# Kernel optimization log

Measured on AMD Instinct MI355X. Metric: run time of the kernel, lower is better.

Reference implementation:

```python
import jax, jax.numpy as jnp
import numpy as np

N, E, D = 100000, 1600000, 128
EPS = 1e-5


def _bn(h, g, b):
    m = h.mean(0)
    v = ((h - m) ** 2).mean(0)  # biased var, as torch BatchNorm1d normalization
    return g * (h - m) / jnp.sqrt(v + EPS) + b


def _sage(x, src, dst, w_self, w_neigh, b, n):
    # mean aggregation over in-neighbors (edges src->dst)
    agg = jax.ops.segment_sum(x[src], dst, num_segments=n)          # [N, D]
    cnt = jax.ops.segment_sum(jnp.ones(src.shape, x.dtype), dst, num_segments=n)
    mean = agg / jnp.maximum(cnt, 1.0)[:, None]
    return x @ w_self + mean @ w_neigh + b


def setup_inputs() -> dict:
    key = jax.random.key(0)
    ks = jax.random.split(key, 8)
    s = 1.0 / np.sqrt(D)
    return {
        "x": jax.random.normal(ks[0], (N, D), jnp.float32),
        "src": jax.random.randint(ks[1], (E,), 0, N, jnp.int32),
        "dst": jax.random.randint(ks[2], (E,), 0, N, jnp.int32),
        "w_self1": jax.random.normal(ks[3], (D, D), jnp.float32) * s,
        "w_neigh1": jax.random.normal(ks[4], (D, D), jnp.float32) * s,
        "b1": jnp.zeros((D,), jnp.float32),
        "w_self2": jax.random.normal(ks[5], (D, D), jnp.float32) * s,
        "w_neigh2": jax.random.normal(ks[6], (D, D), jnp.float32) * s,
        "b2": jnp.zeros((D,), jnp.float32),
        "w_skip": jax.random.normal(ks[7], (D, D), jnp.float32) * s,
        "b_skip": jnp.zeros((D,), jnp.float32),
        "g1": jnp.ones((D,), jnp.float32), "be1": jnp.zeros((D,), jnp.float32),
        "g2": jnp.ones((D,), jnp.float32), "be2": jnp.zeros((D,), jnp.float32),
        "g3": jnp.ones((D,), jnp.float32), "be3": jnp.zeros((D,), jnp.float32),
    }


def reference(x, src, dst, w_self1, w_neigh1, b1, w_self2, w_neigh2, b2,
              w_skip, b_skip, g1, be1, g2, be2, g3, be3):
    n = x.shape[0]
    h1 = _sage(x, src, dst, w_self1, w_neigh1, b1, n)
    h1 = jax.nn.relu(_bn(h1, g1, be1))           # dropout: eval-mode identity
    h2 = _sage(h1, src, dst, w_self2, w_neigh2, b2, n)
    h2 = _bn(h2, g2, be2)
    skip = _bn(h1 @ w_skip + b_skip, g3, be3)
    return jax.nn.relu(h2 + skip)
```

## Files before the change

kernel.cpp:

```cpp
#include <hip/hip_runtime.h>

#define D 128
#define PCHUNK 4096
#define SCAP 8192

typedef short bf16x8 __attribute__((ext_vector_type(8)));
typedef float f32x4 __attribute__((ext_vector_type(4)));
typedef float f32x2 __attribute__((ext_vector_type(2)));

__device__ __forceinline__ ushort f2b(float f){
  unsigned u = __builtin_bit_cast(unsigned, f);
  u += 0x7fffu + ((u >> 16) & 1u);
  return (ushort)(u >> 16);
}
__device__ __forceinline__ float b2f(ushort h){
  unsigned u = ((unsigned)h) << 16;
  return __builtin_bit_cast(float, u);
}
__device__ __forceinline__ f32x2 upk(unsigned u){
  f32x2 r;
  r.x = __builtin_bit_cast(float, u << 16);
  r.y = __builtin_bit_cast(float, u & 0xffff0000u);
  return r;
}

__global__ __launch_bounds__(256) void k_p0(const int* __restrict__ dst,
                                            int* __restrict__ bcnt, int E){
  __shared__ int h[512];
  for (int u=threadIdx.x; u<512; u+=256) h[u]=0;
  __syncthreads();
  for (long long i=(long long)blockIdx.x*256+threadIdx.x; i<E; i+=(long long)gridDim.x*256)
    atomicAdd(&h[dst[i]>>8], 1);
  __syncthreads();
  for (int u=threadIdx.x; u<512; u+=256) if (h[u]) atomicAdd(&bcnt[u], h[u]);
}

__global__ void k_bscan(const int* __restrict__ bcnt, int* __restrict__ bbase,
                        int* __restrict__ bcur, int nb, int E){
  __shared__ int sh[1024];
  int t = threadIdx.x;
  int v = (t<nb) ? bcnt[t] : 0;
  sh[t]=v; __syncthreads();
  for (int off=1; off<1024; off<<=1){
    int add = (t>=off)?sh[t-off]:0;
    __syncthreads();
    sh[t]+=add;
    __syncthreads();
  }
  if (t<nb){ int e=sh[t]-v; bbase[t]=e; bcur[t]=e; }
  if (t==nb) bbase[t]=E;
}

__global__ __launch_bounds__(256) void k_part(const int* __restrict__ src,
        const int* __restrict__ dst, int* __restrict__ bcur,
        unsigned* __restrict__ pairs, int E){
  __shared__ int hist[512], offA[512], offB[512], gbase[512];
  __shared__ int sS[PCHUNK], sD[PCHUNK];
  const int t = threadIdx.x;
  const int base = blockIdx.x * PCHUNK;
  const int cnt = min(PCHUNK, E - base);
  for (int u=t; u<512; u+=256) hist[u]=0;
  __syncthreads();
  int rs[16], rd[16];
  #pragma unroll
  for (int j=0;j<16;j++){
    int li = j*256 + t;
    if (li < cnt){
      rs[j]=src[base+li]; rd[j]=dst[base+li];
      atomicAdd(&hist[rd[j]>>8],1);
    } else { rs[j]=0; rd[j]=-1; }
  }
  __syncthreads();
  int *cur=offA, *nxt=offB;
  for (int u=t; u<512; u+=256) cur[u]=hist[u];
  __syncthreads();
  for (int off=1; off<512; off<<=1){
    for (int u=t; u<512; u+=256) nxt[u] = cur[u] + ((u>=off)?cur[u-off]:0);
    __syncthreads();
    int* tmp=cur; cur=nxt; nxt=tmp;
  }
  for (int u=t; u<512; u+=256) nxt[u] = cur[u]-hist[u];
  __syncthreads();
  #pragma unroll
  for (int j=0;j<16;j++){
    if (j*256+t < cnt){
      int b = rd[j]>>8;
      int p = atomicAdd(&nxt[b],1);
      sS[p]=rs[j]; sD[p]=rd[j];
    }
  }
  __syncthreads();
  for (int u=t; u<512; u+=256){
    int c = hist[u];
    if (c>0) gbase[u] = atomicAdd(&bcur[u], c);
  }
  __syncthreads();
  #pragma unroll
  for (int j=0;j<16;j++){
    int idx = j*256+t;
    if (idx<cnt){
      int d = sD[idx]; int b = d>>8;
      int gpos = gbase[b] + (idx - (cur[b]-hist[b]));
      pairs[gpos] = (unsigned)sS[idx] | ((unsigned)(d & 255) << 24);
    }
  }
}

__global__ __launch_bounds__(256) void k_sortb(const unsigned* __restrict__ pairs,
        const int* __restrict__ bbase, int* __restrict__ offs,
        int* __restrict__ slots, int N, int NB){
  __shared__ int nh[256], nc[256], sc[256];
  __shared__ int stage[SCAP];
  const int b = blockIdx.x, t = threadIdx.x;
  const int base = bbase[b];
  const int cnt  = bbase[b+1] - base;
  nh[t]=0; __syncthreads();
  for (int i=t;i<cnt;i+=256) atomicAdd(&nh[pairs[base+i] >> 24],1);
  __syncthreads();
  int v = nh[t];
  sc[t]=v; __syncthreads();
  for (int off=1; off<256; off<<=1){
    int add = (t>=off)?sc[t-off]:0;
    __syncthreads();
    sc[t]+=add;
    __syncthreads();
  }
  int excl = sc[t]-v;
  nc[t]=excl;
  int node = (b<<8)+t;
  if (node<N) offs[node]=base+excl;
  if (b==NB-1 && t==0) offs[N]=bbase[NB];
  __syncthreads();
  if (cnt<=SCAP){
    for (int i=t;i<cnt;i+=256){
      unsigned p = pairs[base+i];
      int pos = atomicAdd(&nc[p >> 24],1);
      stage[pos]=(int)(p & 0xffffffu);
    }
    __syncthreads();
    for (int i=t;i<cnt;i+=256) slots[base+i]=stage[i];
  } else {
    for (int i=t;i<cnt;i+=256){
      unsigned p = pairs[base+i];
      int pos = atomicAdd(&nc[p >> 24],1);
      slots[base+pos]=(int)(p & 0xffffffu);
    }
  }
}

__global__ __launch_bounds__(256) void k_xcast(const float* __restrict__ x,
                                               ushort* __restrict__ xb, long long n4){
  long long i = (long long)blockIdx.x*256 + threadIdx.x;
  const long long stride = (long long)gridDim.x*256;
  for (; i < n4; i += stride){
    float4 v = reinterpret_cast<const float4*>(x)[i];
    ushort4 o;
    o.x = f2b(v.x); o.y = f2b(v.y); o.z = f2b(v.z); o.w = f2b(v.w);
    reinterpret_cast<ushort4*>(xb)[i] = o;
  }
}

__global__ void k_wt(const float* __restrict__ W, ushort* __restrict__ Wb, int K, int k0){
  int idx = blockIdx.x*256 + threadIdx.x;
  int k = idx >> 7, c = idx & 127;
  Wb[(size_t)c*K + k0 + k] = f2b(W[idx]);
}

__global__ __launch_bounds__(256) void k_gatherb(const ushort* __restrict__ Xb,
        const int* __restrict__ slots, const int* __restrict__ offs,
        ushort* __restrict__ meanb, int N){
  int node = blockIdx.x*4 + (threadIdx.x >> 6);
  const unsigned c2 = (threadIdx.x & 63) * 2;
  if (node >= N) return;
  const int beg = offs[node], end = offs[node+1];
  f32x2 s0{0,0},s1{0,0},s2{0,0},s3{0,0},s4{0,0},s5{0,0},s6{0,0},s7{0,0};
  int j = beg;
  while (j < end && (j & 3)){
    s0 += upk(*reinterpret_cast<const unsigned*>(Xb + ((unsigned)slots[j]*128u + c2)));
    ++j;
  }
  const int nfull = (end - j) >> 3;
  const int4* sp = reinterpret_cast<const int4*>(slots + j);

#define GLD(dstv, idx) dstv = *reinterpret_cast<const unsigned*>(Xb + ((unsigned)(idx)*128u + c2))
#define GATHER8(U, ia, ib) \
    GLD(U##0, (ia).x); GLD(U##1, (ia).y); GLD(U##2, (ia).z); GLD(U##3, (ia).w); \
    GLD(U##4, (ib).x); GLD(U##5, (ib).y); GLD(U##6, (ib).z); GLD(U##7, (ib).w)
#define ACC8(U) \
    s0 += upk(U##0); s1 += upk(U##1); s2 += upk(U##2); s3 += upk(U##3); \
    s4 += upk(U##4); s5 += upk(U##5); s6 += upk(U##6); s7 += upk(U##7)

  unsigned a0,a1,a2,a3,a4,a5,a6,a7;
  unsigned b0,b1,b2,b3,b4,b5,b6,b7;
  if (nfull > 0){
    int4 ia = sp[0], ib = sp[1];
    GATHER8(a, ia, ib);
    int g = 1;
    if (nfull > 1){ ia = sp[2]; ib = sp[3]; }
    for (; g + 1 < nfull; g += 2){
      GATHER8(b, ia, ib);
      ia = sp[2*g+2]; ib = sp[2*g+3];
      ACC8(a);
      GATHER8(a, ia, ib);
      if (g + 2 < nfull){ ia = sp[2*g+4]; ib = sp[2*g+5]; }
      ACC8(b);
    }
    if (g < nfull){
      GATHER8(b, ia, ib);
      ACC8(a);
      ACC8(b);
    } else {
      ACC8(a);
    }
  }
  j += 8*nfull;
  if (end - j >= 4){
    int4 ia = *reinterpret_cast<const int4*>(slots + j);
    unsigned t0,t1,t2,t3;
    GLD(t0, ia.x); GLD(t1, ia.y); GLD(t2, ia.z); GLD(t3, ia.w);
    s0 += upk(t0); s1 += upk(t1); s2 += upk(t2); s3 += upk(t3);
    j += 4;
  }
  for (; j < end; ++j)
    s0 += upk(*reinterpret_cast<const unsigned*>(Xb + ((unsigned)slots[j]*128u + c2)));
#undef GLD
#undef GATHER8
#undef ACC8
  f32x2 s = ((s0+s1)+(s2+s3)) + ((s4+s5)+(s6+s7));
  float deg = (float)(end - beg);
  float rc = deg > 0.f ? 1.0f/deg : 0.f;
  unsigned o = (unsigned)f2b(s.x*rc) | ((unsigned)f2b(s.y*rc) << 16);
  *reinterpret_cast<unsigned*>(meanb + ((size_t)node*D + c2)) = o;
}

template<bool SKIP>
__global__ __launch_bounds__(256, 2) void k_mfma(
    const ushort* __restrict__ A0, const ushort* __restrict__ A1,
    const ushort* __restrict__ Wb, const ushort* __restrict__ Wk,
    const float* __restrict__ bias, const float* __restrict__ biasK,
    ushort* __restrict__ C, ushort* __restrict__ Ck,
    float* __restrict__ gS, float* __restrict__ gQ,
    float* __restrict__ gSK, float* __restrict__ gQK, int N, int NT)
{
  __shared__ ushort At[2][64][40];
  __shared__ ushort Wt[2][128][40];
  __shared__ ushort Wkt[SKIP ? 2*128*40 : 1];
  __shared__ float shS[128], shQ[128], shSK[SKIP?128:1], shQK[SKIP?128:1];
  const int tid = threadIdx.x;
  if (tid < 128){ shS[tid]=0.f; shQ[tid]=0.f; if (SKIP){ shSK[tid]=0.f; shQK[tid]=0.f; } }
  const int bid = blockIdx.x, gridN = gridDim.x;
  const int lane = tid & 63, wid = tid >> 6;
  const int wr = wid >> 1, wc = wid & 1;
  const int lr = lane & 15, kq = lane >> 4;
  const int srA = tid >> 2, s8A = (tid & 3) * 8;
  const int srW = tid >> 2, s8W = (tid & 3) * 8;

  int4 va0, va1, va2, va3;
  int4 w0a,w0b, w1a,w1b, w2a,w2b, w3a,w3b;
  int4 k0a,k0b, k1a,k1b, k2a,k2b, k3a,k3b;

#define LOADSET(S, GT, TT) { \
    int grow_ = (GT)*64 + srA; if (grow_ >= N) grow_ = N-1; \
    const ushort* As_ = ((TT) >= 4) ? A1 : A0; \
    va##S = *reinterpret_cast<const int4*>(&As_[(size_t)grow_*D + ((TT)&3)*32 + s8A]); \
    w##S##a = *reinterpret_cast<const int4*>(&Wb[(size_t)srW*256 + (TT)*32 + s8W]); \
    w##S##b = *reinterpret_cast<const int4*>(&Wb[(size_t)(srW+64)*256 + (TT)*32 + s8W]); \
    if (SKIP && (TT) < 4){ \
      k##S##a = *reinterpret_cast<const int4*>(&Wk[(size_t)srW*128 + (TT)*32 + s8W]); \
      k##S##b = *reinterpret_cast<const int4*>(&Wk[(size_t)(srW+64)*128 + (TT)*32 + s8W]); \
    } }

#define WRITESET(S, BW, TT) { \
    *reinterpret_cast<int4*>(&At[BW][srA][s8A]) = va##S; \
    *reinterpret_cast<int4*>(&Wt[BW][srW][s8W]) = w##S##a; \
    *reinterpret_cast<int4*>(&Wt[BW][srW+64][s8W]) = w##S##b; \
    if (SKIP && (TT) < 4){ \
      *reinterpret_cast<int4*>(&Wkt[((BW)*128 + srW)*40 + s8W]) = k##S##a; \
      *reinterpret_cast<int4*>(&Wkt[((BW)*128 + srW + 64)*40 + s8W]) = k##S##b; \
    } }

#define PBAR() { asm volatile("s_waitcnt lgkmcnt(0)" ::: "memory"); \
    __builtin_amdgcn_s_barrier(); __builtin_amdgcn_sched_barrier(0); }

#define STEPBODY(BR, WITHK, ...) { \
    bf16x8 af0 = *reinterpret_cast<const bf16x8*>(&At[BR][32*wr + lr][kq*8]); \
    bf16x8 af1 = *reinterpret_cast<const bf16x8*>(&At[BR][32*wr + 16 + lr][kq*8]); \
    bf16x8 bw0 = *reinterpret_cast<const bf16x8*>(&Wt[BR][64*wc + lr][kq*8]); \
    bf16x8 bw1 = *reinterpret_cast<const bf16x8*>(&Wt[BR][64*wc + 16 + lr][kq*8]); \
    bf16x8 bw2 = *reinterpret_cast<const bf16x8*>(&Wt[BR][64*wc + 32 + lr][kq*8]); \
    bf16x8 bw3 = *reinterpret_cast<const bf16x8*>(&Wt[BR][64*wc + 48 + lr][kq*8]); \
    bf16x8 bk0{}, bk1{}, bk2{}, bk3{}; \
    if (SKIP && (WITHK)){ \
      bk0 = *reinterpret_cast<const bf16x8*>(&Wkt[((BR)*128 + 64*wc + lr)*40 + kq*8]); \
      bk1 = *reinterpret_cast<const bf16x8*>(&Wkt[((BR)*128 + 64*wc + 16 + lr)*40 + kq*8]); \
      bk2 = *reinterpret_cast<const bf16x8*>(&Wkt[((BR)*128 + 64*wc + 32 + lr)*40 + kq*8]); \
      bk3 = *reinterpret_cast<const bf16x8*>(&Wkt[((BR)*128 + 64*wc + 48 + lr)*40 + kq*8]); \
    } \
    __VA_ARGS__; \
    acc[0][0] = __builtin_amdgcn_mfma_f32_16x16x32_bf16(af0, bw0, acc[0][0], 0,0,0); \
    acc[0][1] = __builtin_amdgcn_mfma_f32_16x16x32_bf16(af0, bw1, acc[0][1], 0,0,0); \
    acc[0][2] = __builtin_amdgcn_mfma_f32_16x16x32_bf16(af0, bw2, acc[0][2], 0,0,0); \
    acc[0][3] = __builtin_amdgcn_mfma_f32_16x16x32_bf16(af0, bw3, acc[0][3], 0,0,0); \
    acc[1][0] = __builtin_amdgcn_mfma_f32_16x16x32_bf16(af1, bw0, acc[1][0], 0,0,0); \
    acc[1][1] = __builtin_amdgcn_mfma_f32_16x16x32_bf16(af1, bw1, acc[1][1], 0,0,0); \
    acc[1][2] = __builtin_amdgcn_mfma_f32_16x16x32_bf16(af1, bw2, acc[1][2], 0,0,0); \
    acc[1][3] = __builtin_amdgcn_mfma_f32_16x16x32_bf16(af1, bw3, acc[1][3], 0,0,0); \
    if (SKIP && (WITHK)){ \
      accK[0][0] = __builtin_amdgcn_mfma_f32_16x16x32_bf16(af0, bk0, accK[0][0], 0,0,0); \
      accK[0][1] = __builtin_amdgcn_mfma_f32_16x16x32_bf16(af0, bk1, accK[0][1], 0,0,0); \
      accK[0][2] = __builtin_amdgcn_mfma_f32_16x16x32_bf16(af0, bk2, accK[0][2], 0,0,0); \
      accK[0][3] = __builtin_amdgcn_mfma_f32_16x16x32_bf16(af0, bk3, accK[0][3], 0,0,0); \
      accK[1][0] = __builtin_amdgcn_mfma_f32_16x16x32_bf16(af1, bk0, accK[1][0], 0,0,0); \
      accK[1][1] = __builtin_amdgcn_mfma_f32_16x16x32_bf16(af1, bk1, accK[1][1], 0,0,0); \
      accK[1][2] = __builtin_amdgcn_mfma_f32_16x16x32_bf16(af1, bk2, accK[1][2], 0,0,0); \
      accK[1][3] = __builtin_amdgcn_mfma_f32_16x16x32_bf16(af1, bk3, accK[1][3], 0,0,0); \
    } }

  f32x4 acc[2][4], accK[SKIP?2:1][SKIP?4:1];
  #pragma unroll
  for (int m=0;m<2;m++)
    #pragma unroll
    for (int n=0;n<4;n++){
      acc[m][n] = (f32x4){0.f,0.f,0.f,0.f};
      if (SKIP) accK[m][n] = (f32x4){0.f,0.f,0.f,0.f};
    }
  float bs[4]={0,0,0,0}, bq[4]={0,0,0,0}, bsk[4]={0,0,0,0}, bqk[4]={0,0,0,0};
  float bv[4], bkv[4];
  #pragma unroll
  for (int n=0;n<4;n++){
    bv[n] = bias[64*wc + 16*n + lr];
    bkv[n] = SKIP ? biasK[64*wc + 16*n + lr] : 0.f;
  }

  {
    const int t0 = bid;
    LOADSET(0, t0, 0);
    LOADSET(1, t0, 1);
    LOADSET(2, t0, 2);
    LOADSET(3, t0, 3);
    WRITESET(0, 0, 0);
    PBAR();
  }

  for (int tile = bid; tile < NT; tile += gridN){
    const int tnext = tile + gridN;
    const bool hasnext = (tnext < NT);
    STEPBODY(0, 1, LOADSET(0, tile, 4));
    WRITESET(1, 1, 1); PBAR();
    STEPBODY(1, 1, LOADSET(1, tile, 5));
    WRITESET(2, 0, 2); PBAR();
    STEPBODY(0, 1, LOADSET(2, tile, 6));
    WRITESET(3, 1, 3); PBAR();
    STEPBODY(1, 1, LOADSET(3, tile, 7));
    WRITESET(0, 0, 4); PBAR();
    STEPBODY(0, 0, if (hasnext) LOADSET(0, tnext, 0));
    WRITESET(1, 1, 5); PBAR();
    STEPBODY(1, 0, if (hasnext) LOADSET(1, tnext, 1));
    WRITESET(2, 0, 6); PBAR();
    STEPBODY(0, 0, if (hasnext) LOADSET(2, tnext, 2));
    WRITESET(3, 1, 7); PBAR();
    STEPBODY(1, 0, if (hasnext) LOADSET(3, tnext, 3));
    if (hasnext){ WRITESET(0, 0, 0); PBAR(); }

    #pragma unroll
    for (int m=0;m<2;m++){
      #pragma unroll
      for (int r=0;r<4;r++){
        int row = tile*64 + 32*wr + 16*m + kq*4 + r;
        if (row < N){
          #pragma unroll
          for (int n=0;n<4;n++){
            int col = 64*wc + 16*n + lr;
            float v = acc[m][n][r] + bv[n];
            C[(size_t)row*D + col] = f2b(v);
            bs[n] += v; bq[n] += v*v;
            if (SKIP){
              float u = accK[m][n][r] + bkv[n];
              Ck[(size_t)row*D + col] = f2b(u);
              bsk[n] += u; bqk[n] += u*u;
            }
          }
        }
      }
    }
    #pragma unroll
    for (int m=0;m<2;m++)
      #pragma unroll
      for (int n=0;n<4;n++){
        acc[m][n] = (f32x4){0.f,0.f,0.f,0.f};
        if (SKIP) accK[m][n] = (f32x4){0.f,0.f,0.f,0.f};
      }
  }
#undef LOADSET
#undef WRITESET
#undef PBAR
#undef STEPBODY

  #pragma unroll
  for (int n=0;n<4;n++){
    float s = bs[n], q = bq[n];
    s += __shfl_xor(s,16); s += __shfl_xor(s,32);
    q += __shfl_xor(q,16); q += __shfl_xor(q,32);
    if (kq == 0){
      int col = 64*wc + 16*n + lr;
      atomicAdd(&shS[col], s);
      atomicAdd(&shQ[col], q);
    }
    if (SKIP){
      float sk = bsk[n], qk = bqk[n];
      sk += __shfl_xor(sk,16); sk += __shfl_xor(sk,32);
      qk += __shfl_xor(qk,16); qk += __shfl_xor(qk,32);
      if (kq == 0){
        int col = 64*wc + 16*n + lr;
        atomicAdd(&shSK[col], sk);
        atomicAdd(&shQK[col], qk);
      }
    }
  }
  __syncthreads();
  if (tid < 128){
    unsafeAtomicAdd(&gS[tid], shS[tid]);
    unsafeAtomicAdd(&gQ[tid], shQ[tid]);
    if (SKIP){
      unsafeAtomicAdd(&gSK[tid], shSK[tid]);
      unsafeAtomicAdd(&gQK[tid], shQK[tid]);
    }
  }
}

__global__ void k_bnfin(const float* __restrict__ sum, const float* __restrict__ sq,
                        const float* __restrict__ g, const float* __restrict__ be,
                        float* __restrict__ bnA, float* __restrict__ bnB, float invN){
  int c = threadIdx.x;
  float m = sum[c]*invN;
  float v = sq[c]*invN - m*m;
  float a = g[c]*rsqrtf(fmaxf(v, 0.f) + 1e-5f);
  bnA[c] = a;
  bnB[c] = be[c] - m*a;
}

__global__ __launch_bounds__(256) void k_bnrelub(const ushort* __restrict__ hpre,
      ushort* __restrict__ hb,
      const float* __restrict__ A, const float* __restrict__ Bp, long long n4){
  long long i = (long long)blockIdx.x*256 + threadIdx.x;
  const long long stride = (long long)gridDim.x*256;
  for (; i < n4; i += stride){
    int c = ((int)(i & 31)) << 2;
    float4 a = *reinterpret_cast<const float4*>(A + c);
    float4 b = *reinterpret_cast<const float4*>(Bp + c);
    ushort4 hv = reinterpret_cast<const ushort4*>(hpre)[i];
    ushort4 o;
    o.x = f2b(fmaxf(a.x*b2f(hv.x) + b.x, 0.f));
    o.y = f2b(fmaxf(a.y*b2f(hv.y) + b.y, 0.f));
    o.z = f2b(fmaxf(a.z*b2f(hv.z) + b.z, 0.f));
    o.w = f2b(fmaxf(a.w*b2f(hv.w) + b.w, 0.f));
    reinterpret_cast<ushort4*>(hb)[i] = o;
  }
}

__global__ __launch_bounds__(256) void k_final(const ushort* __restrict__ h2,
      const ushort* __restrict__ sk, float* __restrict__ out,
      const float* __restrict__ A2, const float* __restrict__ B2,
      const float* __restrict__ A3, const float* __restrict__ B3, long long n4){
  long long i = (long long)blockIdx.x*256 + threadIdx.x;
  const long long stride = (long long)gridDim.x*256;
  for (; i < n4; i += stride){
    int c = ((int)(i & 31)) << 2;
    float4 a2 = *reinterpret_cast<const float4*>(A2 + c);
    float4 b2 = *reinterpret_cast<const float4*>(B2 + c);
    float4 a3 = *reinterpret_cast<const float4*>(A3 + c);
    float4 b3 = *reinterpret_cast<const float4*>(B3 + c);
    ushort4 h = reinterpret_cast<const ushort4*>(h2)[i];
    ushort4 s = reinterpret_cast<const ushort4*>(sk)[i];
    float4 v;
    v.x = fmaxf(a2.x*b2f(h.x) + b2.x + a3.x*b2f(s.x) + b3.x, 0.f);
    v.y = fmaxf(a2.y*b2f(h.y) + b2.y + a3.y*b2f(s.y) + b3.y, 0.f);
    v.z = fmaxf(a2.z*b2f(h.z) + b2.z + a3.z*b2f(s.z) + b3.z, 0.f);
    v.w = fmaxf(a2.w*b2f(h.w) + b2.w + a3.w*b2f(s.w) + b3.w, 0.f);
    reinterpret_cast<float4*>(out)[i] = v;
  }
}

extern "C" void kernel_launch(void* const* d_in, const int* in_sizes, int n_in,
                              void* d_out, int out_size, void* d_ws, size_t ws_size,
                              hipStream_t stream) {
  const float* x        = (const float*)d_in[0];
  const int*   src      = (const int*)  d_in[1];
  const int*   dst      = (const int*)  d_in[2];
  const float* w_self1  = (const float*)d_in[3];
  const float* w_neigh1 = (const float*)d_in[4];
  const float* b1       = (const float*)d_in[5];
  const float* w_self2  = (const float*)d_in[6];
  const float* w_neigh2 = (const float*)d_in[7];
  const float* b2       = (const float*)d_in[8];
  const float* w_skip   = (const float*)d_in[9];
  const float* b_skip   = (const float*)d_in[10];
  const float* g1       = (const float*)d_in[11];
  const float* be1      = (const float*)d_in[12];
  const float* g2       = (const float*)d_in[13];
  const float* be2      = (const float*)d_in[14];
  const float* g3       = (const float*)d_in[15];
  const float* be3      = (const float*)d_in[16];
  (void)n_in; (void)ws_size;

  const int N = in_sizes[0] / D;
  const int E = in_sizes[1];
  const int NB = (N + 255) >> 8;
  float* out = (float*)d_out;

  char* p = (char*)d_ws;
  const size_t nd2 = (((size_t)N * D * 2) + 255) / 256 * 256;
  ushort* meanb  = (ushort*)p; p += nd2;
  ushort* h1b    = (ushort*)p; p += nd2;
  ushort* hpre_b = (ushort*)p; p += nd2;
  ushort* skip_b = (ushort*)p; p += nd2;
  ushort* Wb1    = (ushort*)p; p += 256*128*2;
  ushort* Wb2    = (ushort*)p; p += 256*128*2;
  ushort* Wb3    = (ushort*)p; p += 128*128*2;
  int*    offs   = (int*)p;   p += (((size_t)(N+1)*4) + 255) / 256 * 256;
  int*    bcnt   = (int*)p;   p += 2304;
  float*  st     = (float*)p; p += 1536*sizeof(float);
  int*    bbase  = (int*)p;   p += 2304;
  int*    bcur   = (int*)p;   p += 2048;
  float *sum1=st,      *sq1=st+128,  *sum2=st+256, *sq2=st+384, *sum3=st+512, *sq3=st+640;
  float *bnA1=st+768,  *bnB1=st+896, *bnA2=st+1024,*bnB2=st+1152,*bnA3=st+1280,*bnB3=st+1408;

  const size_t slpad = (((size_t)E*4) + 255) / 256 * 256;
  const size_t xbpad = (((size_t)N*D*2) + 255) / 256 * 256;
  int*      slots = (int*)d_out;
  ushort*   xb    = (ushort*)((char*)d_out + slpad);
  unsigned* pairs = (unsigned*)((char*)d_out + slpad + xbpad);

  hipMemsetAsync(bcnt, 0, 2304 + 1536*sizeof(float), stream);

  const long long n4 = (long long)N * D / 4;

  k_xcast<<<2048, 256, 0, stream>>>(x, xb, n4);
  k_wt<<<64, 256, 0, stream>>>(w_self1,  Wb1, 256, 0);
  k_wt<<<64, 256, 0, stream>>>(w_neigh1, Wb1, 256, 128);
  k_wt<<<64, 256, 0, stream>>>(w_self2,  Wb2, 256, 0);
  k_wt<<<64, 256, 0, stream>>>(w_neigh2, Wb2, 256, 128);
  k_wt<<<64, 256, 0, stream>>>(w_skip,   Wb3, 128, 0);

  k_p0<<<1024, 256, 0, stream>>>(dst, bcnt, E);
  k_bscan<<<1, 1024, 0, stream>>>(bcnt, bbase, bcur, NB, E);
  k_part<<<(E + PCHUNK - 1)/PCHUNK, 256, 0, stream>>>(src, dst, bcur, pairs, E);
  k_sortb<<<NB, 256, 0, stream>>>(pairs, bbase, offs, slots, N, NB);

  const int gablocks = (N + 3) / 4;
  const int NT = (N + 63) / 64;
  const int gpersist = 512;
  const float invN = 1.0f / (float)N;

  k_gatherb<<<gablocks, 256, 0, stream>>>(xb, slots, offs, meanb, N);
  k_mfma<false><<<gpersist, 256, 0, stream>>>(xb, meanb, Wb1, nullptr, b1, nullptr,
                                              hpre_b, nullptr, sum1, sq1, nullptr, nullptr, N, NT);
  k_bnfin<<<1, 128, 0, stream>>>(sum1, sq1, g1, be1, bnA1, bnB1, invN);
  k_bnrelub<<<4096, 256, 0, stream>>>(hpre_b, h1b, bnA1, bnB1, n4);

  k_gatherb<<<gablocks, 256, 0, stream>>>(h1b, slots, offs, meanb, N);

  k_mfma<true><<<gpersist, 256, 0, stream>>>(h1b, meanb, Wb2, Wb3, b2, b_skip,
                                             hpre_b, skip_b, sum2, sq2, sum3, sq3, N, NT);
  k_bnfin<<<1, 128, 0, stream>>>(sum2, sq2, g2, be2, bnA2, bnB2, invN);
  k_bnfin<<<1, 128, 0, stream>>>(sum3, sq3, g3, be3, bnA3, bnB3, invN);

  k_final<<<4096, 256, 0, stream>>>(hpre_b, skip_b, out, bnA2, bnB2, bnA3, bnB3, n4);
}
```

Before: 343.6 us.

## Split neighbor gather across feature slices and edge lanes with shuffle reduction

```diff
diff --git a/kernel.cpp b/kernel.cpp
--- a/kernel.cpp
+++ b/kernel.cpp
@@ -6,7 +6,6 @@
 
 typedef short bf16x8 __attribute__((ext_vector_type(8)));
 typedef float f32x4 __attribute__((ext_vector_type(4)));
-typedef float f32x2 __attribute__((ext_vector_type(2)));
 
 __device__ __forceinline__ ushort f2b(float f){
   unsigned u = __builtin_bit_cast(unsigned, f);
@@ -16,12 +15,6 @@
 __device__ __forceinline__ float b2f(ushort h){
   unsigned u = ((unsigned)h) << 16;
   return __builtin_bit_cast(float, u);
-}
-__device__ __forceinline__ f32x2 upk(unsigned u){
-  f32x2 r;
-  r.x = __builtin_bit_cast(float, u << 16);
-  r.y = __builtin_bit_cast(float, u & 0xffff0000u);
-  return r;
 }
 
 __global__ __launch_bounds__(256) void k_p0(const int* __restrict__ dst,
@@ -169,68 +162,55 @@
 __global__ __launch_bounds__(256) void k_gatherb(const ushort* __restrict__ Xb,
         const int* __restrict__ slots, const int* __restrict__ offs,
         ushort* __restrict__ meanb, int N){
-  int node = blockIdx.x*4 + (threadIdx.x >> 6);
-  const unsigned c2 = (threadIdx.x & 63) * 2;
+  const int slice = blockIdx.x & 7;
+  const int node  = (blockIdx.x >> 3)*4 + (threadIdx.x >> 6);
   if (node >= N) return;
+  const int lane = threadIdx.x & 63;
+  const int e = lane >> 3;
+  const unsigned c2 = slice*16 + (lane & 7)*2;
   const int beg = offs[node], end = offs[node+1];
-  f32x2 s0{0,0},s1{0,0},s2{0,0},s3{0,0},s4{0,0},s5{0,0},s6{0,0},s7{0,0};
+  const int deg = end - beg;
+  float sx = 0.f, sy = 0.f;
   int j = beg;
-  while (j < end && (j & 3)){
-    s0 += upk(*reinterpret_cast<const unsigned*>(Xb + ((unsigned)slots[j]*128u + c2)));
-    ++j;
-  }
-  const int nfull = (end - j) >> 3;
-  const int4* sp = reinterpret_cast<const int4*>(slots + j);
-
-#define GLD(dstv, idx) dstv = *reinterpret_cast<const unsigned*>(Xb + ((unsigned)(idx)*128u + c2))
-#define GATHER8(U, ia, ib) \
-    GLD(U##0, (ia).x); GLD(U##1, (ia).y); GLD(U##2, (ia).z); GLD(U##3, (ia).w); \
-    GLD(U##4, (ib).x); GLD(U##5, (ib).y); GLD(U##6, (ib).z); GLD(U##7, (ib).w)
-#define ACC8(U) \
-    s0 += upk(U##0); s1 += upk(U##1); s2 += upk(U##2); s3 += upk(U##3); \
-    s4 += upk(U##4); s5 += upk(U##5); s6 += upk(U##6); s7 += upk(U##7)
-
-  unsigned a0,a1,a2,a3,a4,a5,a6,a7;
-  unsigned b0,b1,b2,b3,b4,b5,b6,b7;
-  if (nfull > 0){
-    int4 ia = sp[0], ib = sp[1];
-    GATHER8(a, ia, ib);
-    int g = 1;
-    if (nfull > 1){ ia = sp[2]; ib = sp[3]; }
-    for (; g + 1 < nfull; g += 2){
-      GATHER8(b, ia, ib);
-      ia = sp[2*g+2]; ib = sp[2*g+3];
-      ACC8(a);
-      GATHER8(a, ia, ib);
-      if (g + 2 < nfull){ ia = sp[2*g+4]; ib = sp[2*g+5]; }
-      ACC8(b);
-    }
-    if (g < nfull){
-      GATHER8(b, ia, ib);
-      ACC8(a);
-      ACC8(b);
-    } else {
-      ACC8(a);
-    }
-  }
-  j += 8*nfull;
-  if (end - j >= 4){
-    int4 ia = *reinterpret_cast<const int4*>(slots + j);
-    unsigned t0,t1,t2,t3;
-    GLD(t0, ia.x); GLD(t1, ia.y); GLD(t2, ia.z); GLD(t3, ia.w);
-    s0 += upk(t0); s1 += upk(t1); s2 += upk(t2); s3 += upk(t3);
-    j += 4;
-  }
-  for (; j < end; ++j)
-    s0 += upk(*reinterpret_cast<const unsigned*>(Xb + ((unsigned)slots[j]*128u + c2)));
-#undef GLD
-#undef GATHER8
-#undef ACC8
-  f32x2 s = ((s0+s1)+(s2+s3)) + ((s4+s5)+(s6+s7));
-  float deg = (float)(end - beg);
-  float rc = deg > 0.f ? 1.0f/deg : 0.f;
-  unsigned o = (unsigned)f2b(s.x*rc) | ((unsigned)f2b(s.y*rc) << 16);
-  *reinterpret_cast<unsigned*>(meanb + ((size_t)node*D + c2)) = o;
+  int r = deg >> 4;
+  if (r > 0){
+    int i0 = __builtin_nontemporal_load(&slots[j + e]);
+    int i1 = __builtin_nontemporal_load(&slots[j + 8 + e]);
+    for (; r > 1; --r){
+      j += 16;
+      int n0 = __builtin_nontemporal_load(&slots[j + e]);
+      int n1 = __builtin_nontemporal_load(&slots[j + 8 + e]);
+      unsigned u0 = *reinterpret_cast<const unsigned*>(&Xb[(size_t)i0*D + c2]);
+      unsigned u1 = *reinterpret_cast<const unsigned*>(&Xb[(size_t)i1*D + c2]);
+      sx += b2f((ushort)u0); sy += b2f((ushort)(u0>>16));
+      sx += b2f((ushort)u1); sy += b2f((ushort)(u1>>16));
+      i0 = n0; i1 = n1;
+    }
+    unsigned u0 = *reinterpret_cast<const unsigned*>(&Xb[(size_t)i0*D + c2]);
+    unsigned u1 = *reinterpret_cast<const unsigned*>(&Xb[(size_t)i1*D + c2]);
+    sx += b2f((ushort)u0); sy += b2f((ushort)(u0>>16));
+    sx += b2f((ushort)u1); sy += b2f((ushort)(u1>>16));
+    j += 16;
+  }
+  if (j + e < end){
+    int i0 = __builtin_nontemporal_load(&slots[j + e]);
+    unsigned u0 = *reinterpret_cast<const unsigned*>(&Xb[(size_t)i0*D + c2]);
+    sx += b2f((ushort)u0); sy += b2f((ushort)(u0>>16));
+  }
+  if (j + 8 + e < end){
+    int i1 = __builtin_nontemporal_load(&slots[j + 8 + e]);
+    unsigned u1 = *reinterpret_cast<const unsigned*>(&Xb[(size_t)i1*D + c2]);
+    sx += b2f((ushort)u1); sy += b2f((ushort)(u1>>16));
+  }
+  sx += __shfl_xor(sx, 8);  sy += __shfl_xor(sy, 8);
+  sx += __shfl_xor(sx, 16); sy += __shfl_xor(sy, 16);
+  sx += __shfl_xor(sx, 32); sy += __shfl_xor(sy, 32);
+  if (e == 0){
+    float rc = deg > 0 ? 1.0f/(float)deg : 0.f;
+    unsigned o = (unsigned)f2b(sx*rc) | ((unsigned)f2b(sy*rc) << 16);
+    __builtin_nontemporal_store(o,
+        reinterpret_cast<unsigned*>(meanb + (size_t)node*D + c2));
+  }
 }
 
 template<bool SKIP>
@@ -547,7 +527,7 @@
   k_part<<<(E + PCHUNK - 1)/PCHUNK, 256, 0, stream>>>(src, dst, bcur, pairs, E);
   k_sortb<<<NB, 256, 0, stream>>>(pairs, bbase, offs, slots, N, NB);
 
-  const int gablocks = (N + 3) / 4;
+  const int gablocks = ((N + 3) / 4) * 8;
   const int NT = (N + 63) / 64;
   const int gpersist = 512;
   const float invN = 1.0f / (float)N;
```

Result: slower. 768.3 us (+123.6%).
